# Kernel optimization log

Hardware: AMD Instinct MI355X
Metric: run time of the kernel (lower is better)

Reference implementation:

```python
import jax, jax.numpy as jnp
import numpy as np

N_FFT = 2048
HOP = 512
PAD = N_FFT // 2  # 1024, center padding
FREQ_BINS = N_FFT // 2 + 1  # 1025


def _fourier_kernels():
    # freq_scale='no', window='hann' (fftbins=True): w[n] = 0.5 - 0.5*cos(2*pi*n/N)
    s = np.arange(N_FFT, dtype=np.float64)
    win = 0.5 - 0.5 * np.cos(2.0 * np.pi * s / N_FFT)
    k = np.arange(FREQ_BINS, dtype=np.float64)[:, None]
    phase = 2.0 * np.pi * k * s[None, :] / N_FFT  # (freq_bins, n_fft)
    wsin = (win[None, :] * np.sin(phase)).astype(np.float32)
    wcos = (win[None, :] * np.cos(phase)).astype(np.float32)
    return wcos, wsin


def setup_inputs() -> dict:
    key = jax.random.key(0)
    x = jax.random.normal(key, (32, 220500), dtype=jnp.float32)
    wcos, wsin = _fourier_kernels()
    return {"x": x, "wcos": jnp.asarray(wcos), "wsin": jnp.asarray(wsin)}


def reference(x, wcos, wsin):
    # x: (B, L). center=True, pad_mode='reflect'
    xp = jnp.pad(x, ((0, 0), (PAD, PAD)), mode="reflect")[:, None, :]  # (B,1,Lp)
    dn = ("NCH", "OIH", "NCH")
    # one conv with both bases stacked -> (B, 2*freq_bins, T)
    kern = jnp.concatenate([wcos, wsin], axis=0)[:, None, :]  # (2F,1,n_fft)
    spec = jax.lax.conv_general_dilated(
        xp, kern, window_strides=(HOP,), padding="VALID", dimension_numbers=dn
    )
    real, imag = spec[:, :FREQ_BINS, :], spec[:, FREQ_BINS:, :]
    # output_format='Complex': stack (real, -imag) on last axis
    return jnp.stack([real, -imag], axis=-1)  # (B, F, T, 2)
```

## Files before the change

### kernel.cpp

```cpp
#include <hip/hip_runtime.h>
#include <hip/hip_bf16.h>

#define L_IN   220500
#define BATCH  32
#define T_FR   431
#define F_BINS 1025
#define M_TOT  (BATCH * T_FR)
#define KROW   2048
#define WG02   524288
#define WG1    1048576
#define GEMM_BLOCKS 864
#define NYQ_BLOCKS  48
#define BF_BLOCKS   1728
#define WGT_BLOCKS  384

typedef short short8 __attribute__((ext_vector_type(8)));
typedef float floatx4 __attribute__((ext_vector_type(4)));

__device__ __forceinline__ void glds16(const void* g, void* l) {
    __builtin_amdgcn_global_load_lds(
        (const __attribute__((address_space(1))) void*)g,
        (__attribute__((address_space(3))) void*)l, 16, 0, 0);
}

__device__ __forceinline__ short f2bf(float f) {
    __hip_bfloat16 h = __float2bfloat16(f);
    return *reinterpret_cast<short*>(&h);
}

__global__ __launch_bounds__(512) void k_prep(const float* __restrict__ x,
        const float* __restrict__ wcos,
        __hip_bfloat16* __restrict__ yb, __hip_bfloat16* __restrict__ w2) {
    const int blk = blockIdx.x, tid = threadIdx.x;
    if (blk < BF_BLOCKS) {
        int b = blk / 54, rem = blk - b * 54;
        int t = rem * 8 + (tid >> 6);
        if (t >= T_FR) return;
        int q = (tid & 63) * 8;
        const float* xb = x + (size_t)b * L_IN;
        float a[4][8];
        #pragma unroll
        for (int p = 0; p < 4; ++p) {
            const float4* wv = (const float4*)(wcos + 512 * p + q);
            float4 w0 = wv[0], w1 = wv[1];
            float w[8] = {w0.x,w0.y,w0.z,w0.w,w1.x,w1.y,w1.z,w1.w};
            int jb = t * 512 + 512 * p + q - 1024;
            if (jb >= 0 && jb <= L_IN - 8) {
                const float4* s4 = (const float4*)(xb + jb);
                float4 v0 = s4[0], v1 = s4[1];
                float v[8] = {v0.x,v0.y,v0.z,v0.w,v1.x,v1.y,v1.z,v1.w};
                #pragma unroll
                for (int u = 0; u < 8; ++u) a[p][u] = v[u] * w[u];
            } else {
                #pragma unroll
                for (int u = 0; u < 8; ++u) {
                    int j = jb + u;
                    if (j < 0) j = -j;
                    if (j >= L_IN) j = 2 * L_IN - 2 - j;
                    a[p][u] = xb[j] * w[u];
                }
            }
        }
        short8 y0, y2, yre, yim;
        #pragma unroll
        for (int u = 0; u < 8; ++u) {
            y0[u]  = f2bf(a[0][u] + a[1][u] + a[2][u] + a[3][u]);
            y2[u]  = f2bf(a[0][u] - a[1][u] + a[2][u] - a[3][u]);
            yre[u] = f2bf(a[0][u] - a[2][u]);
            yim[u] = f2bf(a[3][u] - a[1][u]);
        }
        short* yr = (short*)yb + (size_t)(b * T_FR + t) * KROW;
        *(short8*)(yr + q)        = y0;
        *(short8*)(yr + 512 + q)  = y2;
        *(short8*)(yr + 1024 + q) = yre;
        *(short8*)(yr + 1536 + q) = yim;
    } else {
        long e0 = (long)(blk - BF_BLOCKS) * 4096 + (long)tid * 8;
        short8 o;
        const float SC = 3.0679615757712823e-3f;
        if (e0 < WG02) {
            int n = (int)(e0 >> 9), q0 = (int)(e0 & 511);
            int c = n & 1;
            int k = (n < 512) ? 4 * (n >> 1) : 4 * ((n - 512) >> 1) + 2;
            #pragma unroll
            for (int u = 0; u < 8; ++u) {
                int ph = (k * (q0 + u)) & 2047;
                float s, cc;
                __sincosf((float)ph * SC, &s, &cc);
                o[u] = f2bf(c ? -s : cc);
            }
        } else {
            long f = e0 - WG02;
            int n = (int)(f >> 10), q0 = (int)(f & 1023);
            int c = n & 1, v = n >> 1;
            int half = q0 >> 9, qq = q0 & 511;
            int k = (v < 256) ? 4 * v + 1 : 3069 - 4 * v;
            #pragma unroll
            for (int u = 0; u < 8; ++u) {
                int ph = (k * (qq + u)) & 2047;
                float s, cc;
                __sincosf((float)ph * SC, &s, &cc);
                float val;
                if (v < 256) val = c ? (half ? cc : -s) : (half ? s : cc);
                else         val = c ? (half ? -cc : s) : (half ? s : cc);
                o[u] = f2bf(val);
            }
        }
        *(short8*)((short*)w2 + e0) = o;
    }
}

#define BARRIER { asm volatile("" ::: "memory"); __builtin_amdgcn_s_barrier(); asm volatile("" ::: "memory"); }
#define VMW(N)  asm volatile("s_waitcnt vmcnt(" #N ")" ::: "memory")
#define SP1     __builtin_amdgcn_s_setprio(1)
#define SP0     __builtin_amdgcn_s_setprio(0)

__global__ __launch_bounds__(512, 2) void k_gemm(
    const __hip_bfloat16* __restrict__ yb,
    const __hip_bfloat16* __restrict__ w2,
    float* __restrict__ out) {

    __shared__ short lds[36864];
    const int tid = threadIdx.x, wave = tid >> 6, lane = tid & 63;

    if (blockIdx.x >= GEMM_BLOCKS) {
        const int gw = (blockIdx.x - GEMM_BLOCKS) * 8 + wave;
        for (int f = gw; f < M_TOT; f += NYQ_BLOCKS * 8) {
            const short* yr = (const short*)yb + (size_t)f * KROW;
            short8 v = *(const short8*)(yr + lane * 8);
            float sum = 0.f;
            #pragma unroll
            for (int u = 0; u < 8; ++u) {
                float e = __uint_as_float(((unsigned)(unsigned short)v[u]) << 16);
                sum += (u & 1) ? -e : e;
            }
            #pragma unroll
            for (int off = 32; off > 0; off >>= 1) sum += __shfl_xor(sum, off);
            if (lane == 0) {
                int b = f / T_FR, t = f - b * T_FR;
                float2 o; o.x = sum; o.y = 0.f;
                ((float2*)out)[((size_t)b * F_BINS + 1024) * T_FR + t] = o;
            }
        }
        return;
    }

    const int bi = blockIdx.x;
    const int bm = (bi & 3) + ((bi >> 5) << 2);
    const int bn = (bi >> 2) & 7;

    const int quad = lane >> 4, l15 = lane & 15;
    const int waveM = wave >> 2, waveN = wave & 3;

    const int g1f   = bn >> 2;
    const int Kg    = g1f ? 1024 : 512;
    const int NTt   = g1f ? 32 : 16;
    const int Koff  = (bn < 2) ? 0 : (bn < 4 ? 512 : 1024);
    const long bbase= g1f ? (long)WG02 + (long)(bn - 4) * 256 * 1024
                          : (long)bn * 256 * 512;
    const int kind  = (bn < 2) ? 0 : (bn < 4 ? 2 : 1);
    const int bnl   = (bn < 2) ? bn : (bn < 4 ? bn - 2 : bn - 4);

    const int l4 = lane >> 2, lc = lane & 3;
    const int swz = (lc ^ ((l4 >> 1) & 3)) * 8;
    int am = bm * 128 + wave * 16 + l4;
    if (am > M_TOT - 1) am = M_TOT - 1;
    const int aoff  = am * KROW + Koff + swz;
    const int brl   = wave * 32 + l4;
    const long boff0 = bbase + (long)brl * Kg + swz;
    const long boff1 = boff0 + (long)16 * Kg;
    const int adst = wave * 512;
    const int bdst = wave * 1024;

    const int rchunk = (quad ^ ((l15 >> 1) & 3)) * 8;
    const int ara = (waveM * 64 + l15) * 32 + rchunk;
    const int bra = (waveN * 64 + l15) * 32 + rchunk;

#define STAGE(BUF, K0) { \
        glds16(yb + aoff  + (K0), &lds[(BUF) * 4096 + adst]); \
        glds16(w2 + boff0 + (K0), &lds[12288 + (BUF) * 8192 + bdst]); \
        glds16(w2 + boff1 + (K0), &lds[12288 + (BUF) * 8192 + bdst + 512]); }

    short8 xf[4], wf[4];
    floatx4 acc[4][4] = {};

    STAGE(0, 0);
    STAGE(1, 32);
    VMW(3);
    BARRIER;

    int r0 = 0, r1 = 1, r2 = 2;
    #pragma unroll 1
    for (int t = 0; t < NTt; ++t) {
        if (t < NTt - 2) STAGE(r2, (t + 2) * 32);
        if (t < NTt - 2)      { VMW(3); }
        else if (t == NTt - 2){ VMW(0); }
        SP1;
        wf[0] = *(const short8*)&lds[12288 + r0 * 8192 + bra];
        #pragma unroll
        for (int j = 0; j < 4; ++j)
            xf[j] = *(const short8*)&lds[r0 * 4096 + ara + j * 512];
        #pragma unroll
        for (int i = 1; i < 4; ++i)
            wf[i] = *(const short8*)&lds[12288 + r0 * 8192 + bra + i * 512];
        #pragma unroll
        for (int i = 0; i < 4; ++i)
            #pragma unroll
            for (int j = 0; j < 4; ++j)
                acc[i][j] = __builtin_amdgcn_mfma_f32_16x16x32_bf16(wf[i], xf[j], acc[i][j], 0, 0, 0);
        SP0;
        if (t < NTt - 1) BARRIER;
        int tmp = r0; r0 = r1; r1 = r2; r2 = tmp;
    }

    float2* __restrict__ out2 = (float2*)out;
    #pragma unroll
    for (int j = 0; j < 4; ++j) {
        int m = bm * 128 + waveM * 64 + j * 16 + l15;
        if (m >= M_TOT) continue;
        int b = m / T_FR, t = m - b * T_FR;
        long tb = (long)b * (F_BINS * T_FR) + t;
        #pragma unroll
        for (int i = 0; i < 4; ++i) {
            #pragma unroll
            for (int p = 0; p < 2; ++p) {
                int pi = bnl * 128 + waveN * 32 + i * 8 + quad * 2 + p;
                int k = (kind == 0) ? 4 * pi
                      : (kind == 2) ? 4 * pi + 2
                      : (pi < 256 ? 4 * pi + 1 : 4 * pi - 1021);
                float2 v; v.x = acc[i][j][2 * p]; v.y = acc[i][j][2 * p + 1];
                out2[tb + (long)k * T_FR] = v;
            }
        }
    }
}

extern "C" void kernel_launch(void* const* d_in, const int* in_sizes, int n_in,
                              void* d_out, int out_size, void* d_ws, size_t ws_size,
                              hipStream_t stream) {
    const float* x    = (const float*)d_in[0];
    const float* wcos = (const float*)d_in[1];
    float* out = (float*)d_out;

    __hip_bfloat16* yb = (__hip_bfloat16*)d_ws;
    __hip_bfloat16* w2 = (__hip_bfloat16*)((char*)d_ws + (size_t)M_TOT * KROW * 2);

    k_prep<<<BF_BLOCKS + WGT_BLOCKS, 512, 0, stream>>>(x, wcos, yb, w2);
    k_gemm<<<GEMM_BLOCKS + NYQ_BLOCKS, 512, 0, stream>>>(yb, w2, out);
}
```

Measured before the change: 223.6 us.

## Pair short-K and long-K GEMM tiles per block to balance work

Each GEMM block now computes two output tiles in sequence: one from the short-K group (512) and one from the long-K group (1024). This halves the block count and gives every block equal total K work, removing the load imbalance between 16-step and 32-step blocks. The wait-count and barrier placement also move so that LDS fragment reads are issued before waiting on the next stage's global-to-LDS loads. The trade-off is fewer blocks in flight, which can leave CUs idle on the tail, plus an extra barrier between the two tiles.

After: 217.1 us. -2.9%, faster.

```diff
diff --git a/kernel.cpp b/kernel.cpp
--- a/kernel.cpp
+++ b/kernel.cpp
@@ -9,7 +9,7 @@
 #define KROW   2048
 #define WG02   524288
 #define WG1    1048576
-#define GEMM_BLOCKS 864
+#define GEMM_BLOCKS 432
 #define NYQ_BLOCKS  48
 #define BF_BLOCKS   1728
 #define WGT_BLOCKS  384
@@ -146,90 +146,96 @@
     }
 
     const int bi = blockIdx.x;
-    const int bm = (bi & 3) + ((bi >> 5) << 2);
-    const int bn = (bi >> 2) & 7;
+    const int j  = (bi >> 2) & 3;
+    const int bm = (bi & 3) + ((bi >> 4) << 2);
 
     const int quad = lane >> 4, l15 = lane & 15;
     const int waveM = wave >> 2, waveN = wave & 3;
-
-    const int g1f   = bn >> 2;
-    const int Kg    = g1f ? 1024 : 512;
-    const int NTt   = g1f ? 32 : 16;
-    const int Koff  = (bn < 2) ? 0 : (bn < 4 ? 512 : 1024);
-    const long bbase= g1f ? (long)WG02 + (long)(bn - 4) * 256 * 1024
-                          : (long)bn * 256 * 512;
-    const int kind  = (bn < 2) ? 0 : (bn < 4 ? 2 : 1);
-    const int bnl   = (bn < 2) ? bn : (bn < 4 ? bn - 2 : bn - 4);
 
     const int l4 = lane >> 2, lc = lane & 3;
     const int swz = (lc ^ ((l4 >> 1) & 3)) * 8;
     int am = bm * 128 + wave * 16 + l4;
     if (am > M_TOT - 1) am = M_TOT - 1;
-    const int aoff  = am * KROW + Koff + swz;
+    const int abase = am * KROW;
     const int brl   = wave * 32 + l4;
-    const long boff0 = bbase + (long)brl * Kg + swz;
-    const long boff1 = boff0 + (long)16 * Kg;
-    const int adst = wave * 512;
-    const int bdst = wave * 1024;
-
+    const int adst  = wave * 512;
+    const int bdst  = wave * 1024;
     const int rchunk = (quad ^ ((l15 >> 1) & 3)) * 8;
     const int ara = (waveM * 64 + l15) * 32 + rchunk;
     const int bra = (waveN * 64 + l15) * 32 + rchunk;
+
+    float2* __restrict__ out2 = (float2*)out;
 
 #define STAGE(BUF, K0) { \
         glds16(yb + aoff  + (K0), &lds[(BUF) * 4096 + adst]); \
         glds16(w2 + boff0 + (K0), &lds[12288 + (BUF) * 8192 + bdst]); \
         glds16(w2 + boff1 + (K0), &lds[12288 + (BUF) * 8192 + bdst + 512]); }
 
-    short8 xf[4], wf[4];
-    floatx4 acc[4][4] = {};
-
-    STAGE(0, 0);
-    STAGE(1, 32);
-    VMW(3);
-    BARRIER;
-
-    int r0 = 0, r1 = 1, r2 = 2;
     #pragma unroll 1
-    for (int t = 0; t < NTt; ++t) {
-        if (t < NTt - 2) STAGE(r2, (t + 2) * 32);
-        if (t < NTt - 2)      { VMW(3); }
-        else if (t == NTt - 2){ VMW(0); }
-        SP1;
-        wf[0] = *(const short8*)&lds[12288 + r0 * 8192 + bra];
+    for (int jj = 0; jj < 2; ++jj) {
+        const int Kg   = jj ? 1024 : 512;
+        const int NTt  = jj ? 32 : 16;
+        const int kind = jj ? 1 : (j < 2 ? 0 : 2);
+        const int Koff = jj ? 1024 : (j < 2 ? 0 : 512);
+        const long bbase = jj ? (long)WG02 + (long)j * 256 * 1024
+                              : (long)j * 256 * 512;
+        const int bnl = jj ? j : (j & 1);
+
+        const int  aoff  = abase + Koff + swz;
+        const long boff0 = bbase + (long)brl * Kg + swz;
+        const long boff1 = boff0 + (long)(16 * Kg);
+
+        short8 xf[4], wf[4];
+        floatx4 acc[4][4] = {};
+
+        if (jj) BARRIER;
+        STAGE(0, 0);
+        STAGE(1, 32);
+        VMW(3);
+        BARRIER;
+
+        int r0 = 0, r1 = 1, r2 = 2;
+        #pragma unroll 1
+        for (int t = 0; t < NTt; ++t) {
+            if (t < NTt - 2) STAGE(r2, (t + 2) * 32);
+            wf[0] = *(const short8*)&lds[12288 + r0 * 8192 + bra];
+            #pragma unroll
+            for (int jm = 0; jm < 4; ++jm)
+                xf[jm] = *(const short8*)&lds[r0 * 4096 + ara + jm * 512];
+            #pragma unroll
+            for (int i = 1; i < 4; ++i)
+                wf[i] = *(const short8*)&lds[12288 + r0 * 8192 + bra + i * 512];
+            SP1;
+            #pragma unroll
+            for (int i = 0; i < 4; ++i)
+                #pragma unroll
+                for (int jm = 0; jm < 4; ++jm)
+                    acc[i][jm] = __builtin_amdgcn_mfma_f32_16x16x32_bf16(wf[i], xf[jm], acc[i][jm], 0, 0, 0);
+            SP0;
+            if (t < NTt - 1) {
+                if (t < NTt - 2) { VMW(3); } else { VMW(0); }
+                BARRIER;
+            }
+            int tmp = r0; r0 = r1; r1 = r2; r2 = tmp;
+        }
+
         #pragma unroll
-        for (int j = 0; j < 4; ++j)
-            xf[j] = *(const short8*)&lds[r0 * 4096 + ara + j * 512];
-        #pragma unroll
-        for (int i = 1; i < 4; ++i)
-            wf[i] = *(const short8*)&lds[12288 + r0 * 8192 + bra + i * 512];
-        #pragma unroll
-        for (int i = 0; i < 4; ++i)
-            #pragma unroll
-            for (int j = 0; j < 4; ++j)
-                acc[i][j] = __builtin_amdgcn_mfma_f32_16x16x32_bf16(wf[i], xf[j], acc[i][j], 0, 0, 0);
-        SP0;
-        if (t < NTt - 1) BARRIER;
-        int tmp = r0; r0 = r1; r1 = r2; r2 = tmp;
-    }
-
-    float2* __restrict__ out2 = (float2*)out;
-    #pragma unroll
-    for (int j = 0; j < 4; ++j) {
-        int m = bm * 128 + waveM * 64 + j * 16 + l15;
-        if (m >= M_TOT) continue;
-        int b = m / T_FR, t = m - b * T_FR;
-        long tb = (long)b * (F_BINS * T_FR) + t;
-        #pragma unroll
-        for (int i = 0; i < 4; ++i) {
-            #pragma unroll
-            for (int p = 0; p < 2; ++p) {
-                int pi = bnl * 128 + waveN * 32 + i * 8 + quad * 2 + p;
-                int k = (kind == 0) ? 4 * pi
-                      : (kind == 2) ? 4 * pi + 2
-                      : (pi < 256 ? 4 * pi + 1 : 4 * pi - 1021);
-                float2 v; v.x = acc[i][j][2 * p]; v.y = acc[i][j][2 * p + 1];
-                out2[tb + (long)k * T_FR] = v;
+        for (int jm = 0; jm < 4; ++jm) {
+            int m = bm * 128 + waveM * 64 + jm * 16 + l15;
+            if (m >= M_TOT) continue;
+            int b = m / T_FR, t = m - b * T_FR;
+            long tb = (long)b * (F_BINS * T_FR) + t;
+            #pragma unroll
+            for (int i = 0; i < 4; ++i) {
+                #pragma unroll
+                for (int p = 0; p < 2; ++p) {
+                    int pi = bnl * 128 + waveN * 32 + i * 8 + quad * 2 + p;
+                    int k = (kind == 0) ? 4 * pi
+                          : (kind == 2) ? 4 * pi + 2
+                          : (pi < 256 ? 4 * pi + 1 : 4 * pi - 1021);
+                    float2 v; v.x = acc[i][jm][2 * p]; v.y = acc[i][jm][2 * p + 1];
+                    out2[tb + (long)k * T_FR] = v;
+                }
             }
         }
     }
```
